# Kernel optimization log

Hardware: AMD Instinct MI355X
Metric: run time of the kernel (lower is better)

Reference implementation:

```python
import jax, jax.numpy as jnp
import numpy as np

DIM, HEADS, MLP_RATIO = 384, 6, 4.0
HEAD_DIM = DIM // HEADS
HID = int(DIM * MLP_RATIO)
EPS = 1e-5


def _layer_norm(x, g, b):
    m = jnp.mean(x, axis=-1, keepdims=True)
    v = jnp.mean(jnp.square(x - m), axis=-1, keepdims=True)
    return (x - m) * jax.lax.rsqrt(v + EPS) * g + b


def setup_inputs() -> dict:
    key = jax.random.key(0)
    ks = jax.random.split(key, 16)
    B, N, C = 4, 2048, DIM
    s = 0.02
    return {
        "x": jax.random.normal(ks[0], (B, N, C), dtype=jnp.float32),
        "ln1_g": jnp.ones((C,), jnp.float32),
        "ln1_b": jnp.zeros((C,), jnp.float32),
        "qkv_w": jax.random.normal(ks[1], (C, 3 * C), jnp.float32) * s,  # [in, out]
        "qkv_b": jnp.zeros((3 * C,), jnp.float32),
        "proj_w": jax.random.normal(ks[2], (C, C), jnp.float32) * s,
        "proj_b": jnp.zeros((C,), jnp.float32),
        "ln2_g": jnp.ones((C,), jnp.float32),
        "ln2_b": jnp.zeros((C,), jnp.float32),
        "fc1_w": jax.random.normal(ks[3], (C, HID), jnp.float32) * s,
        "fc1_b": jnp.zeros((HID,), jnp.float32),
        "fc2_w": jax.random.normal(ks[4], (HID, C), jnp.float32) * s,
        "fc2_b": jnp.zeros((C,), jnp.float32),
    }


def reference(x, ln1_g, ln1_b, qkv_w, qkv_b, proj_w, proj_b,
              ln2_g, ln2_b, fc1_w, fc1_b, fc2_w, fc2_b):
    B, N, C = x.shape
    scale = HEAD_DIM ** (-0.5)

    # --- attention branch (pre-norm) ---
    h = _layer_norm(x, ln1_g, ln1_b)
    qkv = (h @ qkv_w + qkv_b).reshape(B, N, 3, HEADS, HEAD_DIM)
    qkv = jnp.transpose(qkv, (2, 0, 3, 1, 4))  # [3, B, H, N, D]
    q, k, v = qkv[0], qkv[1], qkv[2]
    attn = jnp.einsum("bhnd,bhmd->bhnm", q, k) * scale
    attn = jax.nn.softmax(attn, axis=-1)
    out = jnp.einsum("bhnm,bhmd->bhnd", attn, v)
    out = jnp.transpose(out, (0, 2, 1, 3)).reshape(B, N, C)
    x = x + (out @ proj_w + proj_b)

    # --- MLP branch (pre-norm) ---
    h = _layer_norm(x, ln2_g, ln2_b)
    h = jax.nn.gelu(h @ fc1_w + fc1_b, approximate=False)
    x = x + (h @ fc2_w + fc2_b)
    return x
```

## Files before the change

### kernel.cpp

```cpp
#include <hip/hip_runtime.h>

typedef unsigned short u16;
typedef unsigned int u32;
typedef __bf16 bf16x8_t __attribute__((ext_vector_type(8)));
typedef float f32x4 __attribute__((ext_vector_type(4)));
typedef float f32x16 __attribute__((ext_vector_type(16)));

__device__ __forceinline__ u16 f2b(float f) {
  union { float f; u32 u; } v; v.f = f;
  u32 r = v.u + 0x7fffu + ((v.u >> 16) & 1u);
  return (u16)(r >> 16);
}

__device__ __forceinline__ u32 pkbf(float a, float b) {
  union { __bf16 h[2]; u32 u; } v;
  v.h[0] = (__bf16)a; v.h[1] = (__bf16)b;
  return v.u;
}

__device__ __forceinline__ f32x4 mfma16(uint4 a, uint4 b, f32x4 c) {
  return __builtin_amdgcn_mfma_f32_16x16x32_bf16(
      __builtin_bit_cast(bf16x8_t, a), __builtin_bit_cast(bf16x8_t, b), c, 0, 0, 0);
}

__device__ __forceinline__ f32x16 mfma32(uint4 a, uint4 b, f32x16 c) {
  return __builtin_amdgcn_mfma_f32_32x32x16_bf16(
      __builtin_bit_cast(bf16x8_t, a), __builtin_bit_cast(bf16x8_t, b), c, 0, 0, 0);
}

__device__ __forceinline__ void plswap(u32& a, u32& b) {
  asm("v_permlane32_swap_b32 %0, %1" : "+v"(a), "+v"(b));
}

__device__ __forceinline__ void load_lds16(const void* g, void* l) {
  __builtin_amdgcn_global_load_lds(
      (const __attribute__((address_space(1))) unsigned int*)g,
      (__attribute__((address_space(3))) unsigned int*)l, 16, 0, 0);
}

__device__ __forceinline__ void convT1(const float* w, u16* wt, int K, int N,
                                       int idx) {
  int kk = idx / N, n = idx - kk * N;
  wt[(size_t)n * K + kk] = f2b(w[idx]);
}

__global__ void convT4_k(const float* __restrict__ w0, u16* __restrict__ t0,
                         const float* __restrict__ w1, u16* __restrict__ t1,
                         const float* __restrict__ w2, u16* __restrict__ t2,
                         const float* __restrict__ w3, u16* __restrict__ t3) {
  const int s0 = 384 * 1152, s1 = s0 + 384 * 384, s2 = s1 + 384 * 1536,
            s3 = s2 + 1536 * 384;
  int idx = blockIdx.x * 256 + threadIdx.x;
  if (idx < s0)      convT1(w0, t0, 384, 1152, idx);
  else if (idx < s1) convT1(w1, t1, 384, 384, idx - s0);
  else if (idx < s2) convT1(w2, t2, 384, 1536, idx - s1);
  else if (idx < s3) convT1(w3, t3, 1536, 384, idx - s2);
}

__global__ __launch_bounds__(256) void ln_k(const float* __restrict__ x,
                                            const float* __restrict__ g,
                                            const float* __restrict__ bta,
                                            u16* __restrict__ out) {
  int lane = threadIdx.x & 63, wid = threadIdx.x >> 6;
  int row = blockIdx.x * 4 + wid;
  const float* xr = x + (size_t)row * 384;
  float v[6];
  float s = 0.f;
#pragma unroll
  for (int i = 0; i < 6; i++) { v[i] = xr[i * 64 + lane]; s += v[i]; }
#pragma unroll
  for (int off = 32; off >= 1; off >>= 1) s += __shfl_xor(s, off);
  float mean = s * (1.0f / 384.0f);
  float vs = 0.f;
#pragma unroll
  for (int i = 0; i < 6; i++) { float d = v[i] - mean; vs += d * d; }
#pragma unroll
  for (int off = 32; off >= 1; off >>= 1) vs += __shfl_xor(vs, off);
  float rstd = rsqrtf(vs * (1.0f / 384.0f) + 1e-5f);
  u16* orow = out + (size_t)row * 384;
#pragma unroll
  for (int i = 0; i < 6; i++) {
    int c = i * 64 + lane;
    orow[c] = f2b((v[i] - mean) * rstd * g[c] + bta[c]);
  }
}

template <int EPI, int MR>
__global__ __launch_bounds__(256) void gemm_k(
    const u16* __restrict__ A, const u16* __restrict__ Bt,
    const float* __restrict__ bias, const float* __restrict__ res,
    void* __restrict__ outp, int M, int Nn, int K,
    u16* __restrict__ qp, u16* __restrict__ kp, u16* __restrict__ vtp) {
  constexpr int BMt = MR * 32;
  constexpr int AWV = BMt / 32;
  __shared__ __align__(16) u16 As[2][BMt * 64];
  __shared__ __align__(16) u16 Bs[2][64 * 64];
  int tid = threadIdx.x;
  int lane = tid & 63, wid = tid >> 6;
  int li = lane & 15, lg = lane >> 4;
  int wr = wid >> 1, wc = wid & 1;
  int row0 = blockIdx.y * BMt, col0 = blockIdx.x * 64;

  int lr = lane >> 3;
  int sc8 = ((lane & 7) ^ lr) * 8;

  f32x4 z = {0.f, 0.f, 0.f, 0.f};
  f32x4 acc[MR][2];
#pragma unroll
  for (int m = 0; m < MR; m++)
#pragma unroll
    for (int n = 0; n < 2; n++) acc[m][n] = z;

  auto STAGE = [&](int buf, int k0) {
#pragma unroll
    for (int j = 0; j < AWV; j++) {
      int ia = wid * AWV + j;
      load_lds16(A + (size_t)(row0 + ia * 8 + lr) * K + k0 + sc8,
                 (char*)As[buf] + ia * 1024);
    }
#pragma unroll
    for (int j = 0; j < 2; j++) {
      int ib = wid * 2 + j;
      load_lds16(Bt + (size_t)(col0 + ib * 8 + lr) * K + k0 + sc8,
                 (char*)Bs[buf] + ib * 1024);
    }
  };

  int nsteps = K >> 6;
  STAGE(0, 0);
  asm volatile("s_waitcnt vmcnt(0)");
  __syncthreads();

  int buf = 0;
  for (int t = 0; t < nsteps; t++) {
    if (t + 1 < nsteps) STAGE(buf ^ 1, (t + 1) * 64);
    const char* Asb = (const char*)As[buf];
    const char* Bsb = (const char*)Bs[buf];
#pragma unroll
    for (int kk = 0; kk < 2; kk++) {
      uint4 af[MR], bf[2];
#pragma unroll
      for (int m = 0; m < MR; m++) {
        int r = wr * (MR * 16) + m * 16 + li;
        af[m] = *(const uint4*)(Asb + r * 128 +
                                ((kk * 64 + lg * 16) ^ ((r & 7) << 4)));
      }
#pragma unroll
      for (int n = 0; n < 2; n++) {
        int c = wc * 32 + n * 16 + li;
        bf[n] = *(const uint4*)(Bsb + c * 128 +
                                ((kk * 64 + lg * 16) ^ ((c & 7) << 4)));
      }
#pragma unroll
      for (int m = 0; m < MR; m++)
#pragma unroll
        for (int n = 0; n < 2; n++)
          acc[m][n] = mfma16(af[m], bf[n], acc[m][n]);
    }
    asm volatile("s_waitcnt vmcnt(0)");
    __syncthreads();
    buf ^= 1;
  }

#pragma unroll
  for (int m = 0; m < MR; m++) {
#pragma unroll
    for (int n = 0; n < 2; n++) {
#pragma unroll
      for (int j = 0; j < 4; j++) {
        int r = row0 + wr * (MR * 16) + m * 16 + lg * 4 + j;
        int c = col0 + wc * 32 + n * 16 + li;
        float v = acc[m][n][j] + bias[c];
        if (EPI == 0) {
          ((float*)outp)[(size_t)r * Nn + c] = v + res[(size_t)r * Nn + c];
        } else if (EPI == 1) {
          float gl = 0.5f * v * (1.0f + erff(v * 0.70710678118f));
          ((u16*)outp)[(size_t)r * Nn + c] = f2b(gl);
        } else {
          int t = c / 384;
          int c2 = c - t * 384;
          int hh = c2 >> 6, d = c2 & 63;
          int bb = r >> 11, nn = r & 2047;
          size_t bh = (size_t)bb * 6 + hh;
          int tile = nn >> 5;
          if (t == 2) {
            int kvl = nn & 31;
            int kvHalf = (kvl >> 4) & 1, h2 = (kvl >> 3) & 1, jj = kvl & 7;
            int dTile = d >> 5, l31 = d & 31;
            vtp[(((bh * 64 + tile) * 2 + dTile) * 2 + kvHalf) * 512 +
                (l31 + h2 * 32) * 8 + jj] = f2b(v);
          } else {
            int chunk = d >> 4, h2 = (d >> 3) & 1, e = d & 7;
            int l31 = nn & 31;
            size_t off = ((bh * 64 + tile) * 4 + chunk) * 512 +
                         (l31 + h2 * 32) * 8 + e;
            if (t == 0) qp[off] = f2b(v * 0.125f);
            else        kp[off] = f2b(v);
          }
        }
      }
    }
  }
}

__global__ __launch_bounds__(256, 3) void attn_k(const u16* __restrict__ q,
                                                 const u16* __restrict__ k,
                                                 const u16* __restrict__ vt,
                                                 u16* __restrict__ out) {
  __shared__ __align__(16) float Ol[3][2][16][64];
  __shared__ float Ls[3][64];

  int tid = threadIdx.x;
  int lane = tid & 63, wid = tid >> 6;
  int l31 = lane & 31, hi = lane >> 5;
  int bid = blockIdx.x;
  int nid = (bid & 7) * 192 + (bid >> 3);
  int bh = nid >> 6, qTile = nid & 63;
  int b = bh / 6, hh = bh - b * 6;
  int qb = qTile * 32;

  const u16* qp_ = q + (size_t)(bh * 64 + qTile) * 2048 + lane * 8;
  const u16* kp_ = k + (size_t)(bh * 64 + wid * 16) * 2048 + lane * 8;
  const u16* vp_ = vt + (size_t)(bh * 64 + wid * 16) * 2048 + lane * 8;

  uint4 qf[4], kf[4];
#pragma unroll
  for (int c = 0; c < 4; c++) qf[c] = *(const uint4*)(qp_ + c * 512);
#pragma unroll
  for (int c = 0; c < 4; c++) kf[c] = *(const uint4*)(kp_ + c * 512);
  kp_ += 2048;

  f32x16 o0, o1;
#pragma unroll
  for (int r = 0; r < 16; r++) { o0[r] = 0.f; o1[r] = 0.f; }
  float lsum = 0.f;

#pragma unroll
  for (int t = 0; t < 16; t++) {
    uint4 vf0 = *(const uint4*)(vp_);
    uint4 vf1 = *(const uint4*)(vp_ + 512);
    uint4 vf2 = *(const uint4*)(vp_ + 1024);
    uint4 vf3 = *(const uint4*)(vp_ + 1536);
    uint4 kn[4];
    if (t < 15) {
#pragma unroll
      for (int c = 0; c < 4; c++) kn[c] = *(const uint4*)(kp_ + c * 512);
    }

    f32x16 s;
#pragma unroll
    for (int r = 0; r < 16; r++) s[r] = 0.f;
    s = mfma32(kf[0], qf[0], s);
    s = mfma32(kf[1], qf[1], s);
    s = mfma32(kf[2], qf[2], s);
    s = mfma32(kf[3], qf[3], s);

    float p[16];
#pragma unroll
    for (int r = 0; r < 16; r++) p[r] = __expf(s[r]);

    float a0 = (p[0] + p[1]) + (p[2] + p[3]);
    float a1 = (p[4] + p[5]) + (p[6] + p[7]);
    float a2 = (p[8] + p[9]) + (p[10] + p[11]);
    float a3 = (p[12] + p[13]) + (p[14] + p[15]);
    lsum += (a0 + a1) + (a2 + a3);

    u32 u[8];
#pragma unroll
    for (int i = 0; i < 8; i++) u[i] = pkbf(p[2 * i], p[2 * i + 1]);
    plswap(u[0], u[2]); plswap(u[1], u[3]);
    plswap(u[4], u[6]); plswap(u[5], u[7]);
    uint4 pa0 = {u[0], u[1], u[2], u[3]};
    uint4 pa1 = {u[4], u[5], u[6], u[7]};

    o0 = mfma32(pa0, vf0, o0);
    o0 = mfma32(pa1, vf1, o0);
    o1 = mfma32(pa0, vf2, o1);
    o1 = mfma32(pa1, vf3, o1);

    if (t < 15) {
#pragma unroll
      for (int c = 0; c < 4; c++) kf[c] = kn[c];
    }
    kp_ += 2048;
    vp_ += 2048;
  }

  lsum += __shfl_xor(lsum, 32);

  if (wid) {
#pragma unroll
    for (int r = 0; r < 16; r++) {
      Ol[wid - 1][0][r][lane] = o0[r];
      Ol[wid - 1][1][r][lane] = o1[r];
    }
    Ls[wid - 1][lane] = lsum;
  }
  __syncthreads();
  if (wid == 0) {
#pragma unroll
    for (int w = 0; w < 3; w++) lsum += Ls[w][lane];
#pragma unroll
    for (int r = 0; r < 16; r++)
#pragma unroll
      for (int w = 0; w < 3; w++) {
        o0[r] += Ol[w][0][r][lane];
        o1[r] += Ol[w][1][r][lane];
      }
    float rl = 1.0f / lsum;
#pragma unroll
    for (int r = 0; r < 16; r++) {
      int qo = (r & 3) + 8 * (r >> 2) + hi * 4;
      float rlq = __shfl(rl, qo, 64);
      int row = b * 2048 + qb + qo;
      out[(size_t)row * 384 + hh * 64 + l31] = f2b(o0[r] * rlq);
      out[(size_t)row * 384 + hh * 64 + 32 + l31] = f2b(o1[r] * rlq);
    }
  }
}

extern "C" void kernel_launch(void* const* d_in, const int* in_sizes, int n_in,
                              void* d_out, int out_size, void* d_ws,
                              size_t ws_size, hipStream_t stream) {
  const float* x      = (const float*)d_in[0];
  const float* ln1_g  = (const float*)d_in[1];
  const float* ln1_b  = (const float*)d_in[2];
  const float* qkv_w  = (const float*)d_in[3];
  const float* qkv_b  = (const float*)d_in[4];
  const float* proj_w = (const float*)d_in[5];
  const float* proj_b = (const float*)d_in[6];
  const float* ln2_g  = (const float*)d_in[7];
  const float* ln2_b  = (const float*)d_in[8];
  const float* fc1_w  = (const float*)d_in[9];
  const float* fc1_b  = (const float*)d_in[10];
  const float* fc2_w  = (const float*)d_in[11];
  const float* fc2_b  = (const float*)d_in[12];
  float* out = (float*)d_out;

  char* p = (char*)d_ws;
  u16* qkvwt  = (u16*)p;  p += (size_t)1152 * 384 * 2;
  u16* projwt = (u16*)p;  p += (size_t)384 * 384 * 2;
  u16* fc1wt  = (u16*)p;  p += (size_t)1536 * 384 * 2;
  u16* fc2wt  = (u16*)p;  p += (size_t)384 * 1536 * 2;
  float* x1   = (float*)p; p += (size_t)8192 * 384 * 4;
  u16* reg1   = (u16*)p;  p += (size_t)8192 * 384 * 2;
  u16* reg2   = (u16*)p;  p += (size_t)8192 * 1536 * 2;
  u16* qd  = reg2;
  u16* kd  = reg2 + (size_t)24 * 2048 * 64;
  u16* vtd = kd + (size_t)24 * 2048 * 64;
  u16* h3  = reg2;

  convT4_k<<<6912, 256, 0, stream>>>(qkv_w, qkvwt, proj_w, projwt,
                                     fc1_w, fc1wt, fc2_w, fc2wt);

  ln_k<<<2048, 256, 0, stream>>>(x, ln1_g, ln1_b, reg1);
  gemm_k<2, 4><<<dim3(18, 64), 256, 0, stream>>>(
      reg1, qkvwt, qkv_b, nullptr, nullptr, 8192, 1152, 384, qd, kd, vtd);
  attn_k<<<dim3(1536), 256, 0, stream>>>(qd, kd, vtd, reg1);
  gemm_k<0, 2><<<dim3(6, 128), 256, 0, stream>>>(
      reg1, projwt, proj_b, x, x1, 8192, 384, 384, nullptr, nullptr, nullptr);
  ln_k<<<2048, 256, 0, stream>>>(x1, ln2_g, ln2_b, reg1);
  gemm_k<1, 4><<<dim3(24, 64), 256, 0, stream>>>(
      reg1, fc1wt, fc1_b, nullptr, h3, 8192, 1536, 384, nullptr, nullptr, nullptr);
  gemm_k<0, 2><<<dim3(6, 128), 256, 0, stream>>>(
      h3, fc2wt, fc2_b, x1, out, 8192, 384, 1536, nullptr, nullptr, nullptr);
}
```

Before: 148.0 us.

## Tile weight transpose via LDS, relax GEMM waitcnt, use tanh GELU

The weight conversion now transposes 64x64 tiles through shared memory, so it reads and writes with coalesced vector accesses instead of scattered 2-byte stores. The GEMM main loop waits only for the current stage's loads (partial vmcnt) before a raw barrier, so the prefetch for the next stage can stay in flight during compute. The exact erf GELU in the fc1 epilogue is replaced by a tanh-style approximation written as a sigmoid with __expf. That approximation changes numerics slightly, and the hand-counted vmcnt values have to match the number of loads issued per stage.

```diff
diff --git a/kernel.cpp b/kernel.cpp
--- a/kernel.cpp
+++ b/kernel.cpp
@@ -38,23 +38,39 @@
       (__attribute__((address_space(3))) unsigned int*)l, 16, 0, 0);
 }
 
-__device__ __forceinline__ void convT1(const float* w, u16* wt, int K, int N,
-                                       int idx) {
-  int kk = idx / N, n = idx - kk * N;
-  wt[(size_t)n * K + kk] = f2b(w[idx]);
-}
-
-__global__ void convT4_k(const float* __restrict__ w0, u16* __restrict__ t0,
-                         const float* __restrict__ w1, u16* __restrict__ t1,
-                         const float* __restrict__ w2, u16* __restrict__ t2,
-                         const float* __restrict__ w3, u16* __restrict__ t3) {
-  const int s0 = 384 * 1152, s1 = s0 + 384 * 384, s2 = s1 + 384 * 1536,
-            s3 = s2 + 1536 * 384;
-  int idx = blockIdx.x * 256 + threadIdx.x;
-  if (idx < s0)      convT1(w0, t0, 384, 1152, idx);
-  else if (idx < s1) convT1(w1, t1, 384, 384, idx - s0);
-  else if (idx < s2) convT1(w2, t2, 384, 1536, idx - s1);
-  else if (idx < s3) convT1(w3, t3, 1536, 384, idx - s2);
+__global__ __launch_bounds__(256) void convT4_k(
+    const float* __restrict__ w0, u16* __restrict__ t0_,
+    const float* __restrict__ w1, u16* __restrict__ t1_,
+    const float* __restrict__ w2, u16* __restrict__ t2_,
+    const float* __restrict__ w3, u16* __restrict__ t3_) {
+  __shared__ u16 L[64][68];
+  int tile = blockIdx.x, tid = threadIdx.x;
+  const float* w; u16* wt; int K, N, rel;
+  if (tile < 108)      { w = w0; wt = t0_; K = 384;  N = 1152; rel = tile; }
+  else if (tile < 144) { w = w1; wt = t1_; K = 384;  N = 384;  rel = tile - 108; }
+  else if (tile < 288) { w = w2; wt = t2_; K = 384;  N = 1536; rel = tile - 144; }
+  else                 { w = w3; wt = t3_; K = 1536; N = 384;  rel = tile - 288; }
+  int ntx = N >> 6;
+  int tk = (rel / ntx) << 6, tn = (rel - (rel / ntx) * ntx) << 6;
+
+  int r = tid >> 2, c0 = (tid & 3) << 4;
+  const float* src = w + (size_t)(tk + r) * N + tn + c0;
+#pragma unroll
+  for (int j = 0; j < 16; j += 4) {
+    float4 a = *(const float4*)(src + j);
+    L[r][c0 + j + 0] = f2b(a.x);
+    L[r][c0 + j + 1] = f2b(a.y);
+    L[r][c0 + j + 2] = f2b(a.z);
+    L[r][c0 + j + 3] = f2b(a.w);
+  }
+  __syncthreads();
+  int n = tid >> 2, k0 = (tid & 3) << 4;
+  u16 tmp[16];
+#pragma unroll
+  for (int j = 0; j < 16; j++) tmp[j] = L[k0 + j][n];
+  u16* dst = wt + (size_t)(tn + n) * K + tk + k0;
+  *(uint4*)dst = *(const uint4*)(tmp);
+  *(uint4*)(dst + 8) = *(const uint4*)(tmp + 8);
 }
 
 __global__ __launch_bounds__(256) void ln_k(const float* __restrict__ x,
@@ -128,12 +144,20 @@
 
   int nsteps = K >> 6;
   STAGE(0, 0);
-  asm volatile("s_waitcnt vmcnt(0)");
-  __syncthreads();
 
   int buf = 0;
   for (int t = 0; t < nsteps; t++) {
-    if (t + 1 < nsteps) STAGE(buf ^ 1, (t + 1) * 64);
+    if (t + 1 < nsteps) {
+      STAGE(buf ^ 1, (t + 1) * 64);
+      if constexpr (MR == 4)
+        asm volatile("s_waitcnt vmcnt(6)" ::: "memory");
+      else
+        asm volatile("s_waitcnt vmcnt(4)" ::: "memory");
+    } else {
+      asm volatile("s_waitcnt vmcnt(0)" ::: "memory");
+    }
+    __builtin_amdgcn_s_barrier();
+    asm volatile("" ::: "memory");
     const char* Asb = (const char*)As[buf];
     const char* Bsb = (const char*)Bs[buf];
 #pragma unroll
@@ -157,8 +181,8 @@
         for (int n = 0; n < 2; n++)
           acc[m][n] = mfma16(af[m], bf[n], acc[m][n]);
     }
-    asm volatile("s_waitcnt vmcnt(0)");
-    __syncthreads();
+    asm volatile("" ::: "memory");
+    __builtin_amdgcn_s_barrier();
     buf ^= 1;
   }
 
@@ -174,8 +198,8 @@
         if (EPI == 0) {
           ((float*)outp)[(size_t)r * Nn + c] = v + res[(size_t)r * Nn + c];
         } else if (EPI == 1) {
-          float gl = 0.5f * v * (1.0f + erff(v * 0.70710678118f));
-          ((u16*)outp)[(size_t)r * Nn + c] = f2b(gl);
+          float e = __expf(-1.5957691f * v * (1.f + 0.044715f * v * v));
+          ((u16*)outp)[(size_t)r * Nn + c] = f2b(v / (1.f + e));
         } else {
           int t = c / 384;
           int c2 = c - t * 384;
@@ -350,8 +374,8 @@
   u16* vtd = kd + (size_t)24 * 2048 * 64;
   u16* h3  = reg2;
 
-  convT4_k<<<6912, 256, 0, stream>>>(qkv_w, qkvwt, proj_w, projwt,
-                                     fc1_w, fc1wt, fc2_w, fc2wt);
+  convT4_k<<<432, 256, 0, stream>>>(qkv_w, qkvwt, proj_w, projwt,
+                                    fc1_w, fc1wt, fc2_w, fc2wt);
 
   ln_k<<<2048, 256, 0, stream>>>(x, ln1_g, ln1_b, reg1);
   gemm_k<2, 4><<<dim3(18, 64), 256, 0, stream>>>(
```

After: 140.1 us. 5.3% less time.
